# Kernel optimization log

Measured on AMD Instinct MI355X. Metric: run time of the kernel, lower is better.

Reference implementation:

```python
import jax, jax.numpy as jnp
import numpy as np

N = 100000   # nodes
E = 3200000  # edges
F = 256      # features_size == embedding_size (required by weight2 mm)
EPS = 1e-5   # BatchNorm1d eps


def setup_inputs() -> dict:
    key = jax.random.key(0)
    k1, k2, k3, k4, k5, k6 = jax.random.split(key, 6)
    stdv = 1.0 / np.sqrt(F)
    return {
        "feature": jax.random.normal(k1, (N, F), dtype=jnp.float32),
        "rows": jax.random.randint(k2, (E,), 0, N, dtype=jnp.int32),
        "cols": jax.random.randint(k3, (E,), 0, N, dtype=jnp.int32),
        "vals": jax.random.uniform(k4, (E,), dtype=jnp.float32),
        "W1": jax.random.uniform(k5, (F, F), jnp.float32, -stdv, stdv),
        "W2": jax.random.uniform(k6, (F, F), jnp.float32, -stdv, stdv),
        "gamma": jnp.ones((F,), jnp.float32),
        "beta": jnp.zeros((F,), jnp.float32),
    }


def _spmm_plus_eye(rows, cols, vals, X):
    # (A + I) @ X : gather source features, scale, scatter-add to dest rows, add self-loop
    msgs = vals[:, None] * X[cols]                      # [E, F]
    agg = jax.ops.segment_sum(msgs, rows, num_segments=N)
    return agg + X


def _batchnorm_relu(x, gamma, beta):
    # BatchNorm1d (training-mode batch stats, biased var) + ReLU
    mean = jnp.mean(x, axis=0)
    var = jnp.mean(jnp.square(x - mean), axis=0)
    xn = (x - mean) * jax.lax.rsqrt(var + EPS)
    return jax.nn.relu(xn * gamma + beta)


def reference(feature, rows, cols, vals, W1, W2, gamma, beta):
    support = feature @ W1                              # [N, F]
    out = _spmm_plus_eye(rows, cols, vals, support)     # (A+I) @ support
    out = _batchnorm_relu(out, gamma, beta)
    out = _spmm_plus_eye(rows, cols, vals, out @ W2)    # (A+I) @ (out @ W2)
    return out  # bias=False branch
```

## Files before the change

### kernel.cpp

```cpp
#include <hip/hip_runtime.h>
#include <cstdint>

#define NNODES 100000
#define NEDGES 3200000
#define FEAT   256
#define EPS_BN 1e-5f

#define BSHIFT 9
#define NBUCK  196
#define BCAP   20480
#define PA_BLOCKS 2048
#define PA_CHUNK  1563
#define PA_ITERS  7

__device__ inline unsigned short f2bf(float f) {
  uint32_t u = __float_as_uint(f);
  uint32_t r = (u + 0x7fffu + ((u >> 16) & 1u)) >> 16;
  return (unsigned short)r;
}
__device__ inline float bf2f(unsigned short u) {
  return __uint_as_float(((uint32_t)u) << 16);
}


__global__ void binit_kernel(int* __restrict__ bcur) {
  int i = threadIdx.x;
  if (i < NBUCK) bcur[i] = i * BCAP;
}

__global__ __launch_bounds__(256) void bucketA_kernel(const int* __restrict__ rows,
                                                      const int* __restrict__ cols,
                                                      const float* __restrict__ vals,
                                                      int* __restrict__ bcur,
                                                      int* __restrict__ srow,
                                                      int2* __restrict__ scolval) {
  __shared__ int hist[NBUCK];
  __shared__ int bres[NBUCK];
  __shared__ int cnt2[NBUCK];
  const int tid = threadIdx.x;
  const int c0 = blockIdx.x * PA_CHUNK;
  const int c1 = min(c0 + PA_CHUNK, NEDGES);
  for (int i = tid; i < NBUCK; i += 256) { hist[i] = 0; cnt2[i] = 0; }
  __syncthreads();
  int rr[PA_ITERS], cc[PA_ITERS], bb[PA_ITERS];
  float vv[PA_ITERS];
#pragma unroll
  for (int it = 0; it < PA_ITERS; ++it) {
    int e = c0 + it * 256 + tid;
    bool ok = e < c1;
    rr[it] = ok ? rows[e] : 0;
    cc[it] = ok ? cols[e] : 0;
    vv[it] = ok ? vals[e] : 0.f;
    bb[it] = ok ? (rr[it] >> BSHIFT) : -1;
    if (ok) atomicAdd(&hist[bb[it]], 1);
  }
  __syncthreads();
  if (tid < NBUCK) {
    int x = hist[tid];
    bres[tid] = (x > 0) ? atomicAdd(&bcur[tid], x) : 0;
  }
  __syncthreads();
#pragma unroll
  for (int it = 0; it < PA_ITERS; ++it) {
    if (bb[it] >= 0) {
      int l = atomicAdd(&cnt2[bb[it]], 1);
      int slot = bres[bb[it]] + l;
      srow[slot] = rr[it];
      scolval[slot] = make_int2(cc[it], __float_as_int(vv[it]));
    }
  }
}

__global__ __launch_bounds__(256) void bscan_kernel(const int* __restrict__ bcur,
                                                    int* __restrict__ gbase,
                                                    int* __restrict__ offs_end) {
  __shared__ int wsum[4];
  __shared__ int tot;
  const int tid = threadIdx.x, lane = tid & 63, wid = tid >> 6;
  int x = (tid < NBUCK) ? (bcur[tid] - tid * BCAP) : 0;
  int v = x;
#pragma unroll
  for (int off = 1; off < 64; off <<= 1) {
    int u = __shfl_up(v, off);
    if (lane >= off) v += u;
  }
  if (lane == 63) wsum[wid] = v;
  __syncthreads();
  if (tid == 0) {
    int s = 0;
#pragma unroll
    for (int w = 0; w < 4; ++w) { int t = wsum[w]; wsum[w] = s; s += t; }
    tot = s;
  }
  __syncthreads();
  if (tid < NBUCK) gbase[tid] = v - x + wsum[wid];
  if (tid == 0) *offs_end = tot;
}

__global__ __launch_bounds__(512) void bucketB_kernel(const int* __restrict__ srow,
                                                      const int2* __restrict__ scolval,
                                                      const int* __restrict__ bcur,
                                                      const int* __restrict__ gbase,
                                                      int* __restrict__ offsets,
                                                      int2* __restrict__ edges) {
  __shared__ int hist[512];
  __shared__ int wsum[8];
  const int b = blockIdx.x, tid = threadIdx.x;
  const int r0 = b << BSHIFT;
  const int sbase = b * BCAP;
  const int scount = bcur[b] - sbase;
  const int gb = gbase[b];
  hist[tid] = 0;
  __syncthreads();
  for (int j = tid; j < scount; j += 512)
    atomicAdd(&hist[srow[sbase + j] - r0], 1);
  __syncthreads();
  const int lane = tid & 63, wid = tid >> 6;
  int x = hist[tid], v = x;
#pragma unroll
  for (int off = 1; off < 64; off <<= 1) {
    int u = __shfl_up(v, off);
    if (lane >= off) v += u;
  }
  if (lane == 63) wsum[wid] = v;
  __syncthreads();
  if (tid == 0) {
    int s = 0;
#pragma unroll
    for (int w = 0; w < 8; ++w) { int t = wsum[w]; wsum[w] = s; s += t; }
  }
  __syncthreads();
  int excl = gb + v - x + wsum[wid];
  int r = r0 + tid;
  if (r < NNODES) offsets[r] = excl;
  __syncthreads();
  hist[tid] = excl;
  __syncthreads();
  for (int j = tid; j < scount; j += 512) {
    int lr = srow[sbase + j] - r0;
    int2 cv = scolval[sbase + j];
    int pos = atomicAdd(&hist[lr], 1);
    edges[pos] = cv;
  }
}


template <bool BN>
__global__ __launch_bounds__(256) void gemm_kernel(const float* __restrict__ A,
                                                   const float* __restrict__ B,
                                                   unsigned short* __restrict__ C,
                                                   const float* __restrict__ scale,
                                                   const float* __restrict__ shift) {
  __shared__ float As[16][132];
  __shared__ float Bs[16][132];
  const int tid = threadIdx.x;
  const int row0 = blockIdx.x * 128;
  const int col0 = blockIdx.y * 128;
  const int tr = tid >> 4;
  const int tc = tid & 15;
  float acc[8][8] = {};

  for (int kt = 0; kt < 16; ++kt) {
    __syncthreads();
#pragma unroll
    for (int i = 0; i < 2; ++i) {
      int idx = tid + 256 * i;
      int ar = idx >> 2, ak = idx & 3;
      int grow = row0 + ar;
      float4 av = make_float4(0.f, 0.f, 0.f, 0.f);
      if (grow < NNODES) av = *(const float4*)&A[(size_t)grow * FEAT + kt * 16 + ak * 4];
      if (BN) {
        int kb = kt * 16 + ak * 4;
        float4 sc = *(const float4*)&scale[kb];
        float4 sh = *(const float4*)&shift[kb];
        av.x = fmaxf(0.f, fmaf(av.x, sc.x, sh.x));
        av.y = fmaxf(0.f, fmaf(av.y, sc.y, sh.y));
        av.z = fmaxf(0.f, fmaf(av.z, sc.z, sh.z));
        av.w = fmaxf(0.f, fmaf(av.w, sc.w, sh.w));
      }
      As[ak * 4 + 0][ar] = av.x;
      As[ak * 4 + 1][ar] = av.y;
      As[ak * 4 + 2][ar] = av.z;
      As[ak * 4 + 3][ar] = av.w;
      int bk = idx >> 5, bq = idx & 31;
      float4 bv = *(const float4*)&B[(size_t)(kt * 16 + bk) * FEAT + col0 + bq * 4];
      *(float4*)&Bs[bk][bq * 4] = bv;
    }
    __syncthreads();
#pragma unroll
    for (int k = 0; k < 16; ++k) {
      float a0[8], b0[8];
      *(float4*)&a0[0] = *(const float4*)&As[k][tr * 8];
      *(float4*)&a0[4] = *(const float4*)&As[k][tr * 8 + 4];
      *(float4*)&b0[0] = *(const float4*)&Bs[k][tc * 4];
      *(float4*)&b0[4] = *(const float4*)&Bs[k][64 + tc * 4];
#pragma unroll
      for (int ii = 0; ii < 8; ++ii)
#pragma unroll
        for (int jj = 0; jj < 8; ++jj)
          acc[ii][jj] = fmaf(a0[ii], b0[jj], acc[ii][jj]);
    }
  }
#pragma unroll
  for (int i = 0; i < 8; ++i) {
    int r = row0 + tr * 8 + i;
    if (r < NNODES) {
      ushort4 u0, u1;
      u0.x = f2bf(acc[i][0]); u0.y = f2bf(acc[i][1]);
      u0.z = f2bf(acc[i][2]); u0.w = f2bf(acc[i][3]);
      u1.x = f2bf(acc[i][4]); u1.y = f2bf(acc[i][5]);
      u1.z = f2bf(acc[i][6]); u1.w = f2bf(acc[i][7]);
      *(ushort4*)&C[(size_t)r * FEAT + col0 + tc * 4] = u0;
      *(ushort4*)&C[(size_t)r * FEAT + col0 + 64 + tc * 4] = u1;
    }
  }
}


__global__ __launch_bounds__(256) void spmm_kernel(const unsigned short* __restrict__ X,
                                                   const int* __restrict__ offsets,
                                                   const int2* __restrict__ edges,
                                                   float* __restrict__ Y) {
  const int lane = threadIdx.x & 63;
  const int row = blockIdx.x * 4 + (threadIdx.x >> 6);
  if (row >= NNODES) return;
  const int s = offsets[row], e = offsets[row + 1];
  const ushort4* __restrict__ X4 = (const ushort4*)X;
  float4 acc = make_float4(0.f, 0.f, 0.f, 0.f);
  int j = s;
  for (; j + 4 <= e; j += 4) {
    int2 p0 = edges[j], p1 = edges[j + 1], p2 = edges[j + 2], p3 = edges[j + 3];
    ushort4 x0 = X4[p0.x * 64 + lane];
    ushort4 x1 = X4[p1.x * 64 + lane];
    ushort4 x2 = X4[p2.x * 64 + lane];
    ushort4 x3 = X4[p3.x * 64 + lane];
    float v0 = __int_as_float(p0.y), v1 = __int_as_float(p1.y);
    float v2 = __int_as_float(p2.y), v3 = __int_as_float(p3.y);
    acc.x = fmaf(v0, bf2f(x0.x), acc.x); acc.y = fmaf(v0, bf2f(x0.y), acc.y);
    acc.z = fmaf(v0, bf2f(x0.z), acc.z); acc.w = fmaf(v0, bf2f(x0.w), acc.w);
    acc.x = fmaf(v1, bf2f(x1.x), acc.x); acc.y = fmaf(v1, bf2f(x1.y), acc.y);
    acc.z = fmaf(v1, bf2f(x1.z), acc.z); acc.w = fmaf(v1, bf2f(x1.w), acc.w);
    acc.x = fmaf(v2, bf2f(x2.x), acc.x); acc.y = fmaf(v2, bf2f(x2.y), acc.y);
    acc.z = fmaf(v2, bf2f(x2.z), acc.z); acc.w = fmaf(v2, bf2f(x2.w), acc.w);
    acc.x = fmaf(v3, bf2f(x3.x), acc.x); acc.y = fmaf(v3, bf2f(x3.y), acc.y);
    acc.z = fmaf(v3, bf2f(x3.z), acc.z); acc.w = fmaf(v3, bf2f(x3.w), acc.w);
  }
  for (; j < e; ++j) {
    int2 p = edges[j];
    ushort4 x = X4[p.x * 64 + lane];
    float v = __int_as_float(p.y);
    acc.x = fmaf(v, bf2f(x.x), acc.x); acc.y = fmaf(v, bf2f(x.y), acc.y);
    acc.z = fmaf(v, bf2f(x.z), acc.z); acc.w = fmaf(v, bf2f(x.w), acc.w);
  }
  ushort4 sf = X4[row * 64 + lane];
  acc.x += bf2f(sf.x); acc.y += bf2f(sf.y);
  acc.z += bf2f(sf.z); acc.w += bf2f(sf.w);
  ((float4*)Y)[row * 64 + lane] = acc;
}


__global__ __launch_bounds__(256) void colstats_kernel(const float* __restrict__ X,
                                                       float* __restrict__ sum,
                                                       float* __restrict__ sumsq) {
  const int c = threadIdx.x;
  float s = 0.f, q = 0.f;
  for (int r = blockIdx.x; r < NNODES; r += gridDim.x) {
    float x = X[(size_t)r * FEAT + c];
    s += x;
    q = fmaf(x, x, q);
  }
  atomicAdd(&sum[c], s);
  atomicAdd(&sumsq[c], q);
}

__global__ void bnfinal_kernel(const float* __restrict__ sum, const float* __restrict__ sumsq,
                               const float* __restrict__ gamma, const float* __restrict__ beta,
                               float* __restrict__ scale, float* __restrict__ shift) {
  int c = threadIdx.x;
  float mean = sum[c] * (1.f / NNODES);
  float var = sumsq[c] * (1.f / NNODES) - mean * mean;
  float inv = rsqrtf(var + EPS_BN);
  float sc = gamma[c] * inv;
  scale[c] = sc;
  shift[c] = beta[c] - mean * sc;
}


extern "C" void kernel_launch(void* const* d_in, const int* in_sizes, int n_in,
                              void* d_out, int out_size, void* d_ws, size_t ws_size,
                              hipStream_t stream) {
  const float* feature = (const float*)d_in[0];
  const int*   rows    = (const int*)d_in[1];
  const int*   cols    = (const int*)d_in[2];
  const float* vals    = (const float*)d_in[3];
  const float* W1      = (const float*)d_in[4];
  const float* W2      = (const float*)d_in[5];
  const float* gamma   = (const float*)d_in[6];
  const float* beta    = (const float*)d_in[7];
  float* out = (float*)d_out;

  char* ws = (char*)d_ws;
  size_t nf = (size_t)NNODES * FEAT;
  size_t stagedN = (size_t)NBUCK * BCAP;
  unsigned short* bufBf16 = (unsigned short*)ws;
  int*  srow    = (int*)ws;
  int2* scolval = (int2*)(((uintptr_t)(srow + stagedN) + 15) & ~(uintptr_t)15);
  char* after_shared = ws + ((nf * sizeof(unsigned short) + 255) & ~(size_t)255);
  int2* edges  = (int2*)after_shared;
  int* offsets = (int*)(edges + NEDGES);
  int* bcur    = offsets + (NNODES + 1);
  int* gbase   = bcur + NBUCK;
  float* colsum   = (float*)(gbase + NBUCK);
  float* colsumsq = colsum + FEAT;
  float* bnscale  = colsumsq + FEAT;
  float* bnshift  = bnscale + FEAT;

  hipMemsetAsync(colsum, 0, 2 * FEAT * sizeof(float), stream);

  binit_kernel<<<1, 256, 0, stream>>>(bcur);
  bucketA_kernel<<<PA_BLOCKS, 256, 0, stream>>>(rows, cols, vals, bcur, srow, scolval);
  bscan_kernel<<<1, 256, 0, stream>>>(bcur, gbase, &offsets[NNODES]);
  bucketB_kernel<<<NBUCK, 512, 0, stream>>>(srow, scolval, bcur, gbase, offsets, edges);

  dim3 ggrid((NNODES + 127) / 128, FEAT / 128);
  gemm_kernel<false><<<ggrid, 256, 0, stream>>>(feature, W1, bufBf16, nullptr, nullptr);
  spmm_kernel<<<NNODES / 4, 256, 0, stream>>>(bufBf16, offsets, edges, out);
  colstats_kernel<<<1024, 256, 0, stream>>>(out, colsum, colsumsq);
  bnfinal_kernel<<<1, 256, 0, stream>>>(colsum, colsumsq, gamma, beta, bnscale, bnshift);
  gemm_kernel<true><<<ggrid, 256, 0, stream>>>(out, W2, bufBf16, bnscale, bnshift);
  spmm_kernel<<<NNODES / 4, 256, 0, stream>>>(bufBf16, offsets, edges, out);
}
```

Measured before the change: 1.175 ms.

## Use bf16 MFMA GEMM with pre-transposed weights and wider SpMM edge loads

Replaces the FP32 CUDA-core GEMM with a bf16 MFMA 16x16x32 kernel. Each 512-thread block computes a full 128x256 output tile, with a new prep kernel that transposes W1 and W2 into bf16. The activations are rounded to bf16 before the multiply, which lowers precision. The SpMM now loads two edges per int4 and unrolls 8 edges per iteration to raise memory-level parallelism. The MFMA epilogue writes scalar 16-bit stores, which may be poorly coalesced.

```diff
diff --git a/kernel.cpp b/kernel.cpp
--- a/kernel.cpp
+++ b/kernel.cpp
@@ -13,6 +13,9 @@
 #define PA_CHUNK  1563
 #define PA_ITERS  7
 
+typedef __attribute__((ext_vector_type(8))) short bf16x8;
+typedef __attribute__((ext_vector_type(4))) float f32x4;
+
 __device__ inline unsigned short f2bf(float f) {
   uint32_t u = __float_as_uint(f);
   uint32_t r = (u + 0x7fffu + ((u >> 16) & 1u)) >> 16;
@@ -20,6 +23,9 @@
 }
 __device__ inline float bf2f(unsigned short u) {
   return __uint_as_float(((uint32_t)u) << 16);
+}
+__device__ inline uint32_t pack2(float a, float b) {
+  return (uint32_t)f2bf(a) | ((uint32_t)f2bf(b) << 16);
 }
 
 
@@ -145,77 +151,121 @@
 }
 
 
+__global__ __launch_bounds__(256) void wtprep_kernel(const float* __restrict__ W1,
+                                                     const float* __restrict__ W2,
+                                                     unsigned short* __restrict__ Wt1,
+                                                     unsigned short* __restrict__ Wt2) {
+  const float* W = (blockIdx.x == 0) ? W1 : W2;
+  unsigned short* Wt = (blockIdx.x == 0) ? Wt1 : Wt2;
+  const int n = threadIdx.x;
+  for (int k = 0; k < FEAT; ++k)
+    Wt[n * FEAT + k] = f2bf(W[k * FEAT + n]);
+}
+
+
 template <bool BN>
-__global__ __launch_bounds__(256) void gemm_kernel(const float* __restrict__ A,
-                                                   const float* __restrict__ B,
-                                                   unsigned short* __restrict__ C,
-                                                   const float* __restrict__ scale,
-                                                   const float* __restrict__ shift) {
-  __shared__ float As[16][132];
-  __shared__ float Bs[16][132];
+__global__ __launch_bounds__(512) void gemm_mfma_kernel(const float* __restrict__ A,
+                                                        const unsigned short* __restrict__ Wt,
+                                                        unsigned short* __restrict__ C,
+                                                        const float* __restrict__ scale,
+                                                        const float* __restrict__ shift) {
+  __shared__ unsigned short As[128][40];
+  __shared__ unsigned short Bs[256][40];
   const int tid = threadIdx.x;
+  const int lane = tid & 63;
+  const int wid = tid >> 6;
+  const int wm = wid >> 1;
+  const int wn = wid & 1;
   const int row0 = blockIdx.x * 128;
-  const int col0 = blockIdx.y * 128;
-  const int tr = tid >> 4;
-  const int tc = tid & 15;
-  float acc[8][8] = {};
-
-  for (int kt = 0; kt < 16; ++kt) {
+
+  f32x4 acc[2][8];
+#pragma unroll
+  for (int fm = 0; fm < 2; ++fm)
+#pragma unroll
+    for (int fn = 0; fn < 8; ++fn)
+      acc[fm][fn] = (f32x4){0.f, 0.f, 0.f, 0.f};
+
+  const int arow = lane & 15;
+  const int akb = (lane >> 4) * 8;
+
+  for (int k0 = 0; k0 < FEAT; k0 += 32) {
     __syncthreads();
-#pragma unroll
-    for (int i = 0; i < 2; ++i) {
-      int idx = tid + 256 * i;
-      int ar = idx >> 2, ak = idx & 3;
-      int grow = row0 + ar;
-      float4 av = make_float4(0.f, 0.f, 0.f, 0.f);
-      if (grow < NNODES) av = *(const float4*)&A[(size_t)grow * FEAT + kt * 16 + ak * 4];
+    {
+      int row = tid >> 2, ks = (tid & 3) * 8;
+      int gr = row0 + row;
+      float4 f0 = make_float4(0.f, 0.f, 0.f, 0.f);
+      float4 f1 = make_float4(0.f, 0.f, 0.f, 0.f);
+      if (gr < NNODES) {
+        f0 = *(const float4*)&A[(size_t)gr * FEAT + k0 + ks];
+        f1 = *(const float4*)&A[(size_t)gr * FEAT + k0 + ks + 4];
+      }
       if (BN) {
-        int kb = kt * 16 + ak * 4;
-        float4 sc = *(const float4*)&scale[kb];
-        float4 sh = *(const float4*)&shift[kb];
-        av.x = fmaxf(0.f, fmaf(av.x, sc.x, sh.x));
-        av.y = fmaxf(0.f, fmaf(av.y, sc.y, sh.y));
-        av.z = fmaxf(0.f, fmaf(av.z, sc.z, sh.z));
-        av.w = fmaxf(0.f, fmaf(av.w, sc.w, sh.w));
+        float4 sc0 = *(const float4*)&scale[k0 + ks];
+        float4 sh0 = *(const float4*)&shift[k0 + ks];
+        float4 sc1 = *(const float4*)&scale[k0 + ks + 4];
+        float4 sh1 = *(const float4*)&shift[k0 + ks + 4];
+        f0.x = fmaxf(0.f, fmaf(f0.x, sc0.x, sh0.x));
+        f0.y = fmaxf(0.f, fmaf(f0.y, sc0.y, sh0.y));
+        f0.z = fmaxf(0.f, fmaf(f0.z, sc0.z, sh0.z));
+        f0.w = fmaxf(0.f, fmaf(f0.w, sc0.w, sh0.w));
+        f1.x = fmaxf(0.f, fmaf(f1.x, sc1.x, sh1.x));
+        f1.y = fmaxf(0.f, fmaf(f1.y, sc1.y, sh1.y));
+        f1.z = fmaxf(0.f, fmaf(f1.z, sc1.z, sh1.z));
+        f1.w = fmaxf(0.f, fmaf(f1.w, sc1.w, sh1.w));
       }
-      As[ak * 4 + 0][ar] = av.x;
-      As[ak * 4 + 1][ar] = av.y;
-      As[ak * 4 + 2][ar] = av.z;
-      As[ak * 4 + 3][ar] = av.w;
-      int bk = idx >> 5, bq = idx & 31;
-      float4 bv = *(const float4*)&B[(size_t)(kt * 16 + bk) * FEAT + col0 + bq * 4];
-      *(float4*)&Bs[bk][bq * 4] = bv;
+      uint4 pk;
+      pk.x = pack2(f0.x, f0.y);
+      pk.y = pack2(f0.z, f0.w);
+      pk.z = pack2(f1.x, f1.y);
+      pk.w = pack2(f1.z, f1.w);
+      *(uint4*)&As[row][ks] = pk;
+    }
+    {
+      int n = tid >> 1, ks = (tid & 1) * 16;
+      uint4 w0 = *(const uint4*)&Wt[n * FEAT + k0 + ks];
+      uint4 w1 = *(const uint4*)&Wt[n * FEAT + k0 + ks + 8];
+      *(uint4*)&Bs[n][ks] = w0;
+      *(uint4*)&Bs[n][ks + 8] = w1;
     }
     __syncthreads();
-#pragma unroll
-    for (int k = 0; k < 16; ++k) {
-      float a0[8], b0[8];
-      *(float4*)&a0[0] = *(const float4*)&As[k][tr * 8];
-      *(float4*)&a0[4] = *(const float4*)&As[k][tr * 8 + 4];
-      *(float4*)&b0[0] = *(const float4*)&Bs[k][tc * 4];
-      *(float4*)&b0[4] = *(const float4*)&Bs[k][64 + tc * 4];
-#pragma unroll
-      for (int ii = 0; ii < 8; ++ii)
-#pragma unroll
-        for (int jj = 0; jj < 8; ++jj)
-          acc[ii][jj] = fmaf(a0[ii], b0[jj], acc[ii][jj]);
+
+    bf16x8 af[2], bfr[8];
+#pragma unroll
+    for (int fm = 0; fm < 2; ++fm)
+      af[fm] = *(const bf16x8*)&As[wm * 32 + fm * 16 + arow][akb];
+#pragma unroll
+    for (int fn = 0; fn < 8; ++fn)
+      bfr[fn] = *(const bf16x8*)&Bs[wn * 128 + fn * 16 + arow][akb];
+#pragma unroll
+    for (int fm = 0; fm < 2; ++fm)
+#pragma unroll
+      for (int fn = 0; fn < 8; ++fn)
+        acc[fm][fn] = __builtin_amdgcn_mfma_f32_16x16x32_bf16(af[fm], bfr[fn], acc[fm][fn], 0, 0, 0);
+  }
+
+  const int col = lane & 15;
+  const int r4 = (lane >> 4) * 4;
+#pragma unroll
+  for (int fm = 0; fm < 2; ++fm) {
+#pragma unroll
+    for (int r = 0; r < 4; ++r) {
+      int gr = row0 + wm * 32 + fm * 16 + r4 + r;
+      if (gr < NNODES) {
+#pragma unroll
+        for (int fn = 0; fn < 8; ++fn)
+          C[(size_t)gr * FEAT + wn * 128 + fn * 16 + col] = f2bf(acc[fm][fn][r]);
+      }
     }
   }
-#pragma unroll
-  for (int i = 0; i < 8; ++i) {
-    int r = row0 + tr * 8 + i;
-    if (r < NNODES) {
-      ushort4 u0, u1;
-      u0.x = f2bf(acc[i][0]); u0.y = f2bf(acc[i][1]);
-      u0.z = f2bf(acc[i][2]); u0.w = f2bf(acc[i][3]);
-      u1.x = f2bf(acc[i][4]); u1.y = f2bf(acc[i][5]);
-      u1.z = f2bf(acc[i][6]); u1.w = f2bf(acc[i][7]);
-      *(ushort4*)&C[(size_t)r * FEAT + col0 + tc * 4] = u0;
-      *(ushort4*)&C[(size_t)r * FEAT + col0 + 64 + tc * 4] = u1;
-    }
-  }
-}
-
+}
+
+
+__device__ inline void fma_edge(float4& acc, ushort4 x, float v) {
+  acc.x = fmaf(v, bf2f(x.x), acc.x);
+  acc.y = fmaf(v, bf2f(x.y), acc.y);
+  acc.z = fmaf(v, bf2f(x.z), acc.z);
+  acc.w = fmaf(v, bf2f(x.w), acc.w);
+}
 
 __global__ __launch_bounds__(256) void spmm_kernel(const unsigned short* __restrict__ X,
                                                    const int* __restrict__ offsets,
@@ -226,31 +276,46 @@
   if (row >= NNODES) return;
   const int s = offsets[row], e = offsets[row + 1];
   const ushort4* __restrict__ X4 = (const ushort4*)X;
+  const int4* __restrict__ E2 = (const int4*)edges;
   float4 acc = make_float4(0.f, 0.f, 0.f, 0.f);
   int j = s;
-  for (; j + 4 <= e; j += 4) {
-    int2 p0 = edges[j], p1 = edges[j + 1], p2 = edges[j + 2], p3 = edges[j + 3];
-    ushort4 x0 = X4[p0.x * 64 + lane];
-    ushort4 x1 = X4[p1.x * 64 + lane];
-    ushort4 x2 = X4[p2.x * 64 + lane];
-    ushort4 x3 = X4[p3.x * 64 + lane];
-    float v0 = __int_as_float(p0.y), v1 = __int_as_float(p1.y);
-    float v2 = __int_as_float(p2.y), v3 = __int_as_float(p3.y);
-    acc.x = fmaf(v0, bf2f(x0.x), acc.x); acc.y = fmaf(v0, bf2f(x0.y), acc.y);
-    acc.z = fmaf(v0, bf2f(x0.z), acc.z); acc.w = fmaf(v0, bf2f(x0.w), acc.w);
-    acc.x = fmaf(v1, bf2f(x1.x), acc.x); acc.y = fmaf(v1, bf2f(x1.y), acc.y);
-    acc.z = fmaf(v1, bf2f(x1.z), acc.z); acc.w = fmaf(v1, bf2f(x1.w), acc.w);
-    acc.x = fmaf(v2, bf2f(x2.x), acc.x); acc.y = fmaf(v2, bf2f(x2.y), acc.y);
-    acc.z = fmaf(v2, bf2f(x2.z), acc.z); acc.w = fmaf(v2, bf2f(x2.w), acc.w);
-    acc.x = fmaf(v3, bf2f(x3.x), acc.x); acc.y = fmaf(v3, bf2f(x3.y), acc.y);
-    acc.z = fmaf(v3, bf2f(x3.z), acc.z); acc.w = fmaf(v3, bf2f(x3.w), acc.w);
-  }
-  for (; j < e; ++j) {
+  if ((j & 1) && j < e) {
     int2 p = edges[j];
-    ushort4 x = X4[p.x * 64 + lane];
-    float v = __int_as_float(p.y);
-    acc.x = fmaf(v, bf2f(x.x), acc.x); acc.y = fmaf(v, bf2f(x.y), acc.y);
-    acc.z = fmaf(v, bf2f(x.z), acc.z); acc.w = fmaf(v, bf2f(x.w), acc.w);
+    fma_edge(acc, X4[p.x * 64 + lane], __int_as_float(p.y));
+    ++j;
+  }
+  for (; j + 8 <= e; j += 8) {
+    int4 q0 = E2[(j >> 1) + 0];
+    int4 q1 = E2[(j >> 1) + 1];
+    int4 q2 = E2[(j >> 1) + 2];
+    int4 q3 = E2[(j >> 1) + 3];
+    ushort4 x0 = X4[q0.x * 64 + lane];
+    ushort4 x1 = X4[q0.z * 64 + lane];
+    ushort4 x2 = X4[q1.x * 64 + lane];
+    ushort4 x3 = X4[q1.z * 64 + lane];
+    ushort4 x4 = X4[q2.x * 64 + lane];
+    ushort4 x5 = X4[q2.z * 64 + lane];
+    ushort4 x6 = X4[q3.x * 64 + lane];
+    ushort4 x7 = X4[q3.z * 64 + lane];
+    fma_edge(acc, x0, __int_as_float(q0.y));
+    fma_edge(acc, x1, __int_as_float(q0.w));
+    fma_edge(acc, x2, __int_as_float(q1.y));
+    fma_edge(acc, x3, __int_as_float(q1.w));
+    fma_edge(acc, x4, __int_as_float(q2.y));
+    fma_edge(acc, x5, __int_as_float(q2.w));
+    fma_edge(acc, x6, __int_as_float(q3.y));
+    fma_edge(acc, x7, __int_as_float(q3.w));
+  }
+  for (; j + 2 <= e; j += 2) {
+    int4 q = E2[j >> 1];
+    ushort4 xa = X4[q.x * 64 + lane];
+    ushort4 xb = X4[q.z * 64 + lane];
+    fma_edge(acc, xa, __int_as_float(q.y));
+    fma_edge(acc, xb, __int_as_float(q.w));
+  }
+  if (j < e) {
+    int2 p = edges[j];
+    fma_edge(acc, X4[p.x * 64 + lane], __int_as_float(p.y));
   }
   ushort4 sf = X4[row * 64 + lane];
   acc.x += bf2f(sf.x); acc.y += bf2f(sf.y);
@@ -314,6 +379,8 @@
   float* colsumsq = colsum + FEAT;
   float* bnscale  = colsumsq + FEAT;
   float* bnshift  = bnscale + FEAT;
+  unsigned short* Wt1 = (unsigned short*)(bnshift + FEAT);
+  unsigned short* Wt2 = Wt1 + FEAT * FEAT;
 
   hipMemsetAsync(colsum, 0, 2 * FEAT * sizeof(float), stream);
 
@@ -322,11 +389,13 @@
   bscan_kernel<<<1, 256, 0, stream>>>(bcur, gbase, &offsets[NNODES]);
   bucketB_kernel<<<NBUCK, 512, 0, stream>>>(srow, scolval, bcur, gbase, offsets, edges);
 
-  dim3 ggrid((NNODES + 127) / 128, FEAT / 128);
-  gemm_kernel<false><<<ggrid, 256, 0, stream>>>(feature, W1, bufBf16, nullptr, nullptr);
+  wtprep_kernel<<<2, 256, 0, stream>>>(W1, W2, Wt1, Wt2);
+
+  const int gblocks = (NNODES + 127) / 128;
+  gemm_mfma_kernel<false><<<gblocks, 512, 0, stream>>>(feature, Wt1, bufBf16, nullptr, nullptr);
   spmm_kernel<<<NNODES / 4, 256, 0, stream>>>(bufBf16, offsets, edges, out);
   colstats_kernel<<<1024, 256, 0, stream>>>(out, colsum, colsumsq);
   bnfinal_kernel<<<1, 256, 0, stream>>>(colsum, colsumsq, gamma, beta, bnscale, bnshift);
-  gemm_kernel<true><<<ggrid, 256, 0, stream>>>(out, W2, bufBf16, bnscale, bnshift);
+  gemm_mfma_kernel<true><<<gblocks, 512, 0, stream>>>(out, Wt2, bufBf16, bnscale, bnshift);
   spmm_kernel<<<NNODES / 4, 256, 0, stream>>>(bufBf16, offsets, edges, out);
 }
```

After: 954.0 us. -18.8%, faster.
